# Performance work log

Measured on AMD Instinct MI355X. Metric: run time of the kernel, lower is better.

## Reference

```python
import jax, jax.numpy as jnp
import numpy as np

B, N, TF, DM = 16, 4096, 512, 1024

def next_fast_len(n):
    # smallest 5-smooth number >= n (matches scipy.fftpack.next_fast_len)
    while True:
        m = n
        for p in (2, 3, 5):
            while m % p == 0:
                m //= p
        if m == 1:
            return n
        n += 1

def conv1d_fft(x, weights):
    # x: (..., N, F), weights: (M,); causal exponentially-weighted correlation
    n = x.shape[-2]
    m = weights.shape[-1]
    L = next_fast_len(n + m - 1)
    f_x = jnp.fft.rfft(x, n=L, axis=-2)                 # (..., Lr, F) complex
    f_w = jnp.fft.rfft(weights, n=L, axis=-1)           # (Lr,)
    out = jnp.fft.irfft(f_x * jnp.conj(f_w)[..., None], L, axis=-2)
    out = jnp.roll(out, -1, axis=-2)
    return out[..., L - n:, :]                           # last N along seq axis

def setup_inputs() -> dict:
    key = jax.random.key(0)
    ks = jax.random.split(key, 8)
    inp = {
        "x": jax.random.normal(ks[0], (B, N, TF), dtype=jnp.float32),
        "latent_growth": jax.random.normal(ks[1], (B, N, DM), dtype=jnp.float32),
        "latent_seasonal": jax.random.normal(ks[2], (B, N, DM), dtype=jnp.float32),
        "alpha": jnp.zeros((1,), dtype=jnp.float32),  # nn.Parameter(torch.Tensor([0.0]))
        "w_growth": jax.random.normal(ks[3], (TF, DM), dtype=jnp.float32) / np.sqrt(DM),
        "b_growth": jnp.zeros((TF,), dtype=jnp.float32),
        "w_seasonal": jax.random.normal(ks[4], (TF, DM), dtype=jnp.float32) / np.sqrt(DM),
        "b_seasonal": jnp.zeros((TF,), dtype=jnp.float32),
    }
    return inp

def reference(x, latent_growth, latent_seasonal, alpha, w_growth, b_growth, w_seasonal, b_seasonal):
    n = x.shape[1]
    a = jax.nn.sigmoid(alpha)[0]
    powers = jnp.arange(n, dtype=x.dtype)[::-1]          # flipped arange
    seasonal = jnp.einsum('bnd,fd->bnf', latent_seasonal, w_seasonal) + b_seasonal
    aes_weights = a * (1.0 - a) ** powers                # alpha*(1-alpha)^k EMA kernel
    seasonal_normalized_term = conv1d_fft(x - seasonal, aes_weights)
    # NOTE: the original module computes `growth` but does not use it in the output
    growth = jnp.einsum('bnd,fd->bnf', latent_growth, w_growth) + b_growth
    growth_term = conv1d_fft(x, aes_weights)
    return seasonal_normalized_term + growth_term
```

## Files before the change

kernel.cpp:

```cpp
#include <hip/hip_runtime.h>
#include <math.h>

#define B_DIM 16
#define N_SEQ 4096
#define TF_DIM 512
#define DM_DIM 1024
#define CHUNK 128
#define NCHUNK (N_SEQ / CHUNK)
#define NT 16

typedef __attribute__((ext_vector_type(4))) float f32x4;
typedef __attribute__((ext_vector_type(8))) short bf16x8;
typedef unsigned short u16;
typedef unsigned int u32;

__device__ __forceinline__ u16 f2bf(float f) {
    u32 u = __builtin_bit_cast(u32, f);
    u += 0x7fffu + ((u >> 16) & 1u);
    return (u16)(u >> 16);
}

__device__ __forceinline__ u32 cvtpk(float lo, float hi) {
    u32 r;
    asm("v_cvt_pk_bf16_f32 %0, %1, %2" : "=v"(r) : "v"(lo), "v"(hi));
    return r;
}

__device__ __forceinline__ void gload16(const u16* g, u16* l) {
    __builtin_amdgcn_global_load_lds(
        (const __attribute__((address_space(1))) void*)g,
        (__attribute__((address_space(3))) void*)l, 16, 0, 0);
}

#define BAR() __builtin_amdgcn_s_barrier()
#define SYNC_DRAIN() asm volatile("s_waitcnt vmcnt(0)\n\ts_barrier" ::: "memory")

__global__ __launch_bounds__(256)
void cvt_bf16(const float* __restrict__ ls, const float* __restrict__ wm,
              u16* __restrict__ lsb, u16* __restrict__ wmb)
{
    const size_t LSG = (size_t)B_DIM * N_SEQ * DM_DIM / 4;
    const size_t i = (size_t)blockIdx.x * 256 + threadIdx.x;
    const float* src;
    u16* dst;
    if (i < LSG) { src = ls + i * 4; dst = lsb + i * 4; }
    else         { const size_t j = i - LSG; src = wm + j * 4; dst = wmb + j * 4; }
    const f32x4 v = *(const f32x4*)src;
    u32* d = (u32*)dst;
    d[0] = cvtpk(v[0], v[1]);
    d[1] = cvtpk(v[2], v[3]);
}

__global__ __launch_bounds__(512, 2)
void gemm_u_kernel(const float* __restrict__ x,
                   const u16* __restrict__ lsb,
                   const u16* __restrict__ wmb,
                   const float* __restrict__ bias,
                   const float* __restrict__ alpha,
                   u16* __restrict__ u,
                   float* __restrict__ e)
{
    __shared__ u16 As[2][2][8192];
    __shared__ u16 Ws[2][2][8192];

    const int tid = threadIdx.x;

    const int s  = blockIdx.x;
    const int kk = s >> 3;
    const int fb = kk & 1;
    const int rp = (s & 7) + ((kk >> 1) << 3);
    const int f0   = fb * 256;
    const int row0 = rp * 256;

    const int lane = tid & 63;
    const int wid  = tid >> 6;
    const int wm = wid >> 2;
    const int wn = wid & 3;
    const int wh = wn >> 1, wlo = wn & 1;
    const int l15 = lane & 15, l4 = lane >> 4;

    const int g0 = wid * 128 + lane;
    const int g1 = g0 + 64;
    const int r0 = ((g0 >> 7) << 4) | ((g0 >> 2) & 15);
    const int c0 = (((g0 >> 6) & 1) << 5) | ((((g0 & 3) ^ (((g0 >> 5) & 1) << 1))) << 3);
    const int r1 = ((g1 >> 7) << 4) | ((g1 >> 2) & 15);
    const int c1 = (((g1 >> 6) & 1) << 5) | ((((g1 & 3) ^ (((g1 >> 5) & 1) << 1))) << 3);
    const int dst0 = wid * 1024;
    const int dst1 = wid * 1024 + 512;

    const u16* pa0 = lsb + (size_t)(row0 + r0) * DM_DIM + c0;
    const u16* pa1 = lsb + (size_t)(row0 + r1) * DM_DIM + c1;
    const u16* pw0 = wmb + (size_t)(f0 + r0) * DM_DIM + c0;
    const u16* pw1 = wmb + (size_t)(f0 + r1) * DM_DIM + c1;
    const size_t H = (size_t)128 * DM_DIM;

    const int com = (l15 << 5) | ((l4 << 3) ^ (((l15 >> 3) & 1) << 4));

    f32x4 acc[8][4];
#pragma unroll
    for (int i = 0; i < 8; ++i)
#pragma unroll
        for (int j = 0; j < 4; ++j) acc[i][j] = (f32x4){0.f, 0.f, 0.f, 0.f};

#define STAGE_A(NB, T) do {                                               \
        gload16(pa0 + (size_t)(T) * 64,     &As[NB][0][dst0]);            \
        gload16(pa1 + (size_t)(T) * 64,     &As[NB][0][dst1]);            \
        gload16(pa0 + (size_t)(T) * 64 + H, &As[NB][1][dst0]);            \
        gload16(pa1 + (size_t)(T) * 64 + H, &As[NB][1][dst1]);            \
    } while (0)
#define STAGE_W(NB, T) do {                                               \
        gload16(pw0 + (size_t)(T) * 64,     &Ws[NB][0][dst0]);            \
        gload16(pw1 + (size_t)(T) * 64,     &Ws[NB][0][dst1]);            \
        gload16(pw0 + (size_t)(T) * 64 + H, &Ws[NB][1][dst0]);            \
        gload16(pw1 + (size_t)(T) * 64 + H, &Ws[NB][1][dst1]);            \
    } while (0)

#define PHASE(BUF, MIH, KS) do {                                          \
        const u16* _Ab = &As[BUF][wm][0];                                 \
        const u16* _Wb = &Ws[BUF][wh][0];                                 \
        bf16x8 _af[4], _wf[4];                                            \
        _Pragma("unroll")                                                 \
        for (int q = 0; q < 4; ++q)                                       \
            _af[q] = *(const bf16x8*)(_Ab + (((MIH)*4 + q) << 10)         \
                                          + ((KS) << 9) + com);           \
        _Pragma("unroll")                                                 \
        for (int n = 0; n < 4; ++n)                                       \
            _wf[n] = *(const bf16x8*)(_Wb + ((wlo*4 + n) << 10)           \
                                          + ((KS) << 9) + com);           \
        __builtin_amdgcn_s_setprio(1);                                    \
        _Pragma("unroll")                                                 \
        for (int q = 0; q < 4; ++q)                                       \
        _Pragma("unroll")                                                 \
        for (int n = 0; n < 4; ++n)                                       \
            acc[(MIH)*4 + q][n] = __builtin_amdgcn_mfma_f32_16x16x32_bf16(\
                _af[q], _wf[n], acc[(MIH)*4 + q][n], 0, 0, 0);            \
        __builtin_amdgcn_s_setprio(0);                                    \
    } while (0)

    STAGE_A(0, 0);
    STAGE_W(0, 0);
    SYNC_DRAIN();

#pragma unroll 1
    for (int t = 0; t < NT; ++t) {
        const int bt = t & 1;
        const int nb = bt ^ 1;
        if (t + 1 < NT) STAGE_A(nb, t + 1);
        PHASE(bt, 0, 0);
        BAR();
        if (t + 1 < NT) STAGE_W(nb, t + 1);
        PHASE(bt, 0, 1);
        BAR();
        PHASE(bt, 1, 0);
        BAR();
        PHASE(bt, 1, 1);
        SYNC_DRAIN();
    }

    const float a = 1.0f / (1.0f + expf(-alpha[0]));
    const float c = 1.0f - a;
    const float l2c = log2f(c);

    float bia[4];
#pragma unroll
    for (int ni = 0; ni < 4; ++ni) bia[ni] = bias[f0 + wn * 64 + ni * 16 + l15];

    float epart[4] = {0.f, 0.f, 0.f, 0.f};

#pragma unroll
    for (int mi = 0; mi < 8; ++mi) {
#pragma unroll
        for (int j = 0; j < 4; ++j) {
            const int rc = mi * 16 + l4 * 4 + j;
            const int r  = wm * 128 + rc;
            const size_t rb = (size_t)(row0 + r) * TF_DIM;
            const float wgt = (rc == CHUNK - 1)
                                  ? a
                                  : a * exp2f((float)(CHUNK - 1 - rc) * l2c);
#pragma unroll
            for (int ni = 0; ni < 4; ++ni) {
                const int f = f0 + wn * 64 + ni * 16 + l15;
                const float uval = 2.0f * x[rb + f] - (acc[mi][ni][j] + bia[ni]);
                u[rb + f] = f2bf(uval);
                epart[ni] = fmaf(wgt, uval, epart[ni]);
            }
        }
    }

#pragma unroll
    for (int ni = 0; ni < 4; ++ni) {
        epart[ni] += __shfl_xor(epart[ni], 16, 64);
        epart[ni] += __shfl_xor(epart[ni], 32, 64);
    }
    if (l4 == 0) {
#pragma unroll
        for (int ni = 0; ni < 4; ++ni) {
            const int f = f0 + wn * 64 + ni * 16 + l15;
            e[(size_t)(rp * 2 + wm) * TF_DIM + f] = epart[ni];
        }
    }
}

__global__ __launch_bounds__(256)
void ema_carry(const float* __restrict__ e, const float* __restrict__ alpha,
               float* __restrict__ carry)
{
    const int idx = blockIdx.x * 256 + threadIdx.x;
    const int f = idx & (TF_DIM - 1);
    const int b = idx >> 9;
    const float a = 1.0f / (1.0f + expf(-alpha[0]));
    const float c = 1.0f - a;
    const float cC = exp2f((float)CHUNK * log2f(c));
    const size_t base = (size_t)b * NCHUNK * TF_DIM + f;
    float Y = 0.0f;
    carry[base] = 0.0f;
    for (int ch = 1; ch < NCHUNK; ++ch) {
        Y = fmaf(cC, Y, e[base + (size_t)(ch - 1) * TF_DIM]);
        carry[base + (size_t)ch * TF_DIM] = Y;
    }
}

__global__ __launch_bounds__(256)
void ema_apply(const u16* __restrict__ u, const float* __restrict__ carry,
               const float* __restrict__ alpha, float* __restrict__ out)
{
    const int bc = blockIdx.x;
    const int tid = threadIdx.x;
    const float a = 1.0f / (1.0f + expf(-alpha[0]));
    const float c = 1.0f - a;
    float y0 = carry[(size_t)bc * TF_DIM + 2 * tid];
    float y1 = carry[(size_t)bc * TF_DIM + 2 * tid + 1];
    const u32* up = (const u32*)(u + (size_t)bc * CHUNK * TF_DIM) + tid;
    float2*    op = (float2*)(out + (size_t)bc * CHUNK * TF_DIM) + tid;
#pragma unroll 4
    for (int j = 0; j < CHUNK; ++j) {
        const u32 w = up[(size_t)j * (TF_DIM / 2)];
        const float u0 = __builtin_bit_cast(float, (w & 0xffffu) << 16);
        const float u1 = __builtin_bit_cast(float, (w >> 16) << 16);
        y0 = fmaf(c, y0, a * u0);
        y1 = fmaf(c, y1, a * u1);
        op[(size_t)j * (TF_DIM / 2)] = make_float2(y0, y1);
    }
}

extern "C" void kernel_launch(void* const* d_in, const int* in_sizes, int n_in,
                              void* d_out, int out_size, void* d_ws, size_t ws_size,
                              hipStream_t stream) {
    const float* x     = (const float*)d_in[0];
    const float* ls    = (const float*)d_in[2];
    const float* alpha = (const float*)d_in[3];
    const float* wmat  = (const float*)d_in[6];
    const float* bias  = (const float*)d_in[7];
    float* out = (float*)d_out;

    u16*   u     = (u16*)d_ws;
    u16*   lsb   = u + (size_t)B_DIM * N_SEQ * TF_DIM;
    u16*   wmb   = lsb + (size_t)B_DIM * N_SEQ * DM_DIM;
    float* e     = (float*)(wmb + (size_t)TF_DIM * DM_DIM);
    float* carry = e + (size_t)B_DIM * NCHUNK * TF_DIM;

    const int cvt_blocks = (B_DIM * N_SEQ * DM_DIM / 4 + TF_DIM * DM_DIM / 4) / 256;
    cvt_bf16<<<cvt_blocks, 256, 0, stream>>>(ls, wmat, lsb, wmb);

    gemm_u_kernel<<<512, 512, 0, stream>>>(x, lsb, wmb, bias, alpha, u, e);

    ema_carry<<<(B_DIM * TF_DIM) / 256, 256, 0, stream>>>(e, alpha, carry);
    ema_apply<<<B_DIM * NCHUNK, 256, 0, stream>>>(u, carry, alpha, out);
}
```

Before: 247.5 us.

## Pre-tile bf16 operands into swizzled blocks and use a 4-stage K pipeline

The conversion kernel now writes latent and weight bf16 data into a pre-tiled, XOR-swizzled layout of 256x32 K-slices, so each GEMM block loads contiguous 16KB tiles. The GEMM loop switches from a double-buffered K=64 schedule with several barriers per step to a 4-buffer ring of K=32 slices, keeping up to three slices in flight and using partial vmcnt waits with one barrier per step. The aim is to hide global-to-LDS latency and cut barrier stalls, at the cost of more K iterations, a more complex pack kernel and a changed workspace layout.

```diff
diff --git a/kernel.cpp b/kernel.cpp
--- a/kernel.cpp
+++ b/kernel.cpp
@@ -7,7 +7,7 @@
 #define DM_DIM 1024
 #define CHUNK 128
 #define NCHUNK (N_SEQ / CHUNK)
-#define NT 16
+#define NT 32
 
 typedef __attribute__((ext_vector_type(4))) float f32x4;
 typedef __attribute__((ext_vector_type(8))) short bf16x8;
@@ -32,23 +32,43 @@
         (__attribute__((address_space(3))) void*)l, 16, 0, 0);
 }
 
-#define BAR() __builtin_amdgcn_s_barrier()
-#define SYNC_DRAIN() asm volatile("s_waitcnt vmcnt(0)\n\ts_barrier" ::: "memory")
+#define WAIT8_BAR() asm volatile("s_waitcnt vmcnt(8)\n\ts_barrier" ::: "memory")
+#define WAIT4_BAR() asm volatile("s_waitcnt vmcnt(4)\n\ts_barrier" ::: "memory")
+#define WAIT0_BAR() asm volatile("s_waitcnt vmcnt(0)\n\ts_barrier" ::: "memory")
 
 __global__ __launch_bounds__(256)
-void cvt_bf16(const float* __restrict__ ls, const float* __restrict__ wm,
-              u16* __restrict__ lsb, u16* __restrict__ wmb)
-{
-    const size_t LSG = (size_t)B_DIM * N_SEQ * DM_DIM / 4;
+void pack_bf16(const float* __restrict__ ls, const float* __restrict__ wmat,
+               u16* __restrict__ lsb, u16* __restrict__ wmb)
+{
+    const size_t LSG = (size_t)B_DIM * N_SEQ * 128;
     const size_t i = (size_t)blockIdx.x * 256 + threadIdx.x;
     const float* src;
     u16* dst;
-    if (i < LSG) { src = ls + i * 4; dst = lsb + i * 4; }
-    else         { const size_t j = i - LSG; src = wm + j * 4; dst = wmb + j * 4; }
-    const f32x4 v = *(const f32x4*)src;
+    if (i < LSG) {
+        const int srow = (int)(i >> 7);
+        const int sg   = (int)(i & 127);
+        const int t = sg >> 2, g = sg & 3;
+        const int rp = srow >> 8, row = srow & 255;
+        const int gp = g ^ (row & 3) ^ ((row >> 2) & 3);
+        src = ls + ((size_t)srow << 10) + sg * 8;
+        dst = lsb + (((size_t)(rp * 32 + t)) << 13) + row * 32 + gp * 8;
+    } else {
+        const size_t j = i - LSG;
+        const int srow = (int)(j >> 7);
+        const int sg   = (int)(j & 127);
+        const int t = sg >> 2, g = sg & 3;
+        const int fb = srow >> 8, row = srow & 255;
+        const int gp = g ^ (row & 3) ^ ((row >> 2) & 3);
+        src = wmat + ((size_t)srow << 10) + sg * 8;
+        dst = wmb + (((size_t)(fb * 32 + t)) << 13) + row * 32 + gp * 8;
+    }
+    const f32x4 v0 = *(const f32x4*)src;
+    const f32x4 v1 = *(const f32x4*)(src + 4);
     u32* d = (u32*)dst;
-    d[0] = cvtpk(v[0], v[1]);
-    d[1] = cvtpk(v[2], v[3]);
+    d[0] = cvtpk(v0[0], v0[1]);
+    d[1] = cvtpk(v0[2], v0[3]);
+    d[2] = cvtpk(v1[0], v1[1]);
+    d[3] = cvtpk(v1[2], v1[3]);
 }
 
 __global__ __launch_bounds__(512, 2)
@@ -60,8 +80,8 @@
                    u16* __restrict__ u,
                    float* __restrict__ e)
 {
-    __shared__ u16 As[2][2][8192];
-    __shared__ u16 Ws[2][2][8192];
+    __shared__ u16 As[4][8192];
+    __shared__ u16 Ws[4][8192];
 
     const int tid = threadIdx.x;
 
@@ -76,25 +96,32 @@
     const int wid  = tid >> 6;
     const int wm = wid >> 2;
     const int wn = wid & 3;
-    const int wh = wn >> 1, wlo = wn & 1;
     const int l15 = lane & 15, l4 = lane >> 4;
 
-    const int g0 = wid * 128 + lane;
-    const int g1 = g0 + 64;
-    const int r0 = ((g0 >> 7) << 4) | ((g0 >> 2) & 15);
-    const int c0 = (((g0 >> 6) & 1) << 5) | ((((g0 & 3) ^ (((g0 >> 5) & 1) << 1))) << 3);
-    const int r1 = ((g1 >> 7) << 4) | ((g1 >> 2) & 15);
-    const int c1 = (((g1 >> 6) & 1) << 5) | ((((g1 & 3) ^ (((g1 >> 5) & 1) << 1))) << 3);
-    const int dst0 = wid * 1024;
-    const int dst1 = wid * 1024 + 512;
-
-    const u16* pa0 = lsb + (size_t)(row0 + r0) * DM_DIM + c0;
-    const u16* pa1 = lsb + (size_t)(row0 + r1) * DM_DIM + c1;
-    const u16* pw0 = wmb + (size_t)(f0 + r0) * DM_DIM + c0;
-    const u16* pw1 = wmb + (size_t)(f0 + r1) * DM_DIM + c1;
-    const size_t H = (size_t)128 * DM_DIM;
-
-    const int com = (l15 << 5) | ((l4 << 3) ^ (((l15 >> 3) & 1) << 4));
+    const u16* pa = lsb + ((size_t)rp << 18);
+    const u16* pw = wmb + ((size_t)fb << 18);
+    const int qa   = (wid * 128 + lane) * 8;
+    const int ldsb = wid * 1024;
+
+#define STG(NB, T) do {                                                   \
+        const size_t _b = ((size_t)(T)) << 13;                            \
+        gload16(pa + _b + qa,       &As[NB][ldsb]);                       \
+        gload16(pa + _b + qa + 512, &As[NB][ldsb + 512]);                 \
+        gload16(pw + _b + qa,       &Ws[NB][ldsb]);                       \
+        gload16(pw + _b + qa + 512, &Ws[NB][ldsb + 512]);                 \
+    } while (0)
+
+    int rofa[8], rofw[4];
+#pragma unroll
+    for (int mi = 0; mi < 8; ++mi) {
+        const int ra = wm * 128 + mi * 16 + l15;
+        rofa[mi] = ra * 32 + ((l4 ^ (ra & 3) ^ ((ra >> 2) & 3)) * 8);
+    }
+#pragma unroll
+    for (int ni = 0; ni < 4; ++ni) {
+        const int rw = wn * 64 + ni * 16 + l15;
+        rofw[ni] = rw * 32 + ((l4 ^ (rw & 3) ^ ((rw >> 2) & 3)) * 8);
+    }
 
     f32x4 acc[8][4];
 #pragma unroll
@@ -102,60 +129,40 @@
 #pragma unroll
         for (int j = 0; j < 4; ++j) acc[i][j] = (f32x4){0.f, 0.f, 0.f, 0.f};
 
-#define STAGE_A(NB, T) do {                                               \
-        gload16(pa0 + (size_t)(T) * 64,     &As[NB][0][dst0]);            \
-        gload16(pa1 + (size_t)(T) * 64,     &As[NB][0][dst1]);            \
-        gload16(pa0 + (size_t)(T) * 64 + H, &As[NB][1][dst0]);            \
-        gload16(pa1 + (size_t)(T) * 64 + H, &As[NB][1][dst1]);            \
-    } while (0)
-#define STAGE_W(NB, T) do {                                               \
-        gload16(pw0 + (size_t)(T) * 64,     &Ws[NB][0][dst0]);            \
-        gload16(pw1 + (size_t)(T) * 64,     &Ws[NB][0][dst1]);            \
-        gload16(pw0 + (size_t)(T) * 64 + H, &Ws[NB][1][dst0]);            \
-        gload16(pw1 + (size_t)(T) * 64 + H, &Ws[NB][1][dst1]);            \
-    } while (0)
-
-#define PHASE(BUF, MIH, KS) do {                                          \
-        const u16* _Ab = &As[BUF][wm][0];                                 \
-        const u16* _Wb = &Ws[BUF][wh][0];                                 \
-        bf16x8 _af[4], _wf[4];                                            \
-        _Pragma("unroll")                                                 \
-        for (int q = 0; q < 4; ++q)                                       \
-            _af[q] = *(const bf16x8*)(_Ab + (((MIH)*4 + q) << 10)         \
-                                          + ((KS) << 9) + com);           \
-        _Pragma("unroll")                                                 \
-        for (int n = 0; n < 4; ++n)                                       \
-            _wf[n] = *(const bf16x8*)(_Wb + ((wlo*4 + n) << 10)           \
-                                          + ((KS) << 9) + com);           \
+#define COMPUTE(BUF) do {                                                 \
+        const u16* _Ab = As[BUF];                                         \
+        const u16* _Wb = Ws[BUF];                                         \
+        bf16x8 _af[8], _wf[4];                                            \
+        _Pragma("unroll")                                                 \
+        for (int mi = 0; mi < 8; ++mi)                                    \
+            _af[mi] = *(const bf16x8*)(_Ab + rofa[mi]);                   \
+        _Pragma("unroll")                                                 \
+        for (int ni = 0; ni < 4; ++ni)                                    \
+            _wf[ni] = *(const bf16x8*)(_Wb + rofw[ni]);                   \
         __builtin_amdgcn_s_setprio(1);                                    \
         _Pragma("unroll")                                                 \
-        for (int q = 0; q < 4; ++q)                                       \
-        _Pragma("unroll")                                                 \
-        for (int n = 0; n < 4; ++n)                                       \
-            acc[(MIH)*4 + q][n] = __builtin_amdgcn_mfma_f32_16x16x32_bf16(\
-                _af[q], _wf[n], acc[(MIH)*4 + q][n], 0, 0, 0);            \
+        for (int mi = 0; mi < 8; ++mi)                                    \
+        _Pragma("unroll")                                                 \
+        for (int ni = 0; ni < 4; ++ni)                                    \
+            acc[mi][ni] = __builtin_amdgcn_mfma_f32_16x16x32_bf16(        \
+                _af[mi], _wf[ni], acc[mi][ni], 0, 0, 0);                  \
         __builtin_amdgcn_s_setprio(0);                                    \
     } while (0)
 
-    STAGE_A(0, 0);
-    STAGE_W(0, 0);
-    SYNC_DRAIN();
+    STG(0, 0);
+    STG(1, 1);
+    STG(2, 2);
 
 #pragma unroll 1
-    for (int t = 0; t < NT; ++t) {
-        const int bt = t & 1;
-        const int nb = bt ^ 1;
-        if (t + 1 < NT) STAGE_A(nb, t + 1);
-        PHASE(bt, 0, 0);
-        BAR();
-        if (t + 1 < NT) STAGE_W(nb, t + 1);
-        PHASE(bt, 0, 1);
-        BAR();
-        PHASE(bt, 1, 0);
-        BAR();
-        PHASE(bt, 1, 1);
-        SYNC_DRAIN();
-    }
+    for (int t = 0; t < NT - 2; ++t) {
+        WAIT8_BAR();
+        if (t + 3 < NT) STG((t + 3) & 3, t + 3);
+        COMPUTE(t & 3);
+    }
+    WAIT4_BAR();
+    COMPUTE(2);
+    WAIT0_BAR();
+    COMPUTE(3);
 
     const float a = 1.0f / (1.0f + expf(-alpha[0]));
     const float c = 1.0f - a;
@@ -256,11 +263,11 @@
     u16*   u     = (u16*)d_ws;
     u16*   lsb   = u + (size_t)B_DIM * N_SEQ * TF_DIM;
     u16*   wmb   = lsb + (size_t)B_DIM * N_SEQ * DM_DIM;
-    float* e     = (float*)(wmb + (size_t)TF_DIM * DM_DIM);
+    float* e     = (float*)(wmb + (size_t)2 * 32 * 8192);
     float* carry = e + (size_t)B_DIM * NCHUNK * TF_DIM;
 
-    const int cvt_blocks = (B_DIM * N_SEQ * DM_DIM / 4 + TF_DIM * DM_DIM / 4) / 256;
-    cvt_bf16<<<cvt_blocks, 256, 0, stream>>>(ls, wmat, lsb, wmb);
+    const int pack_blocks = (B_DIM * N_SEQ * 128 + 512 * 128) / 256;
+    pack_bf16<<<pack_blocks, 256, 0, stream>>>(ls, wmat, lsb, wmb);
 
     gemm_u_kernel<<<512, 512, 0, stream>>>(x, lsb, wmb, bias, alpha, u, e);
 
```

Result: slower. 268.9 us (+8.6%).
